# Optimization experiments

Hardware: AMD Instinct MI355X
Metric: run time of the kernel (lower is better)

Reference implementation:

```python
import jax, jax.numpy as jnp
import numpy as np

N_HEAD, D_MODEL, D_K, D_V = 8, 128, 16, 16
EPS = 1e-5


def entmax15(x):
    # 1.5-entmax along last axis (Peters & Martins 2019, exact sort-based algo)
    x = x * 0.5
    x = x - jnp.max(x, axis=-1, keepdims=True)
    xs = jnp.flip(jnp.sort(x, axis=-1), axis=-1)  # descending
    K = x.shape[-1]
    rho = jnp.arange(1, K + 1, dtype=x.dtype)
    mean = jnp.cumsum(xs, axis=-1) / rho
    mean_sq = jnp.cumsum(xs * xs, axis=-1) / rho
    delta = (1.0 - rho * (mean_sq - mean * mean)) / rho
    tau = mean - jnp.sqrt(jnp.clip(delta, 0.0))
    support = jnp.sum(tau <= xs, axis=-1, keepdims=True)  # support size k*
    tau_star = jnp.take_along_axis(tau, support - 1, axis=-1)
    p = jnp.clip(x - tau_star, 0.0)
    return p * p


def layer_norm(x, gamma, beta):
    mu = jnp.mean(x, axis=-1, keepdims=True)
    var = jnp.mean((x - mu) ** 2, axis=-1, keepdims=True)
    return gamma * (x - mu) * jax.lax.rsqrt(var + EPS) + beta


def setup_inputs() -> dict:
    key = jax.random.key(0)
    ks = jax.random.split(key, 24)
    B, Lq, Lk, D = 4, 1024, 2048, D_MODEL
    s = 0.05
    f = jax.random.normal
    return {
        "q": f(ks[0], (B, Lq, D), jnp.float32),
        "k": f(ks[1], (B, Lk, D), jnp.float32),
        "v": f(ks[2], (B, Lk, D), jnp.float32),
        "v_2": f(ks[3], (B, Lq, D), jnp.float32),
        "W_Q": f(ks[4], (D, N_HEAD * D_K)) * s, "b_Q": f(ks[5], (N_HEAD * D_K,)) * s,
        "W_K": f(ks[6], (D, N_HEAD * D_K)) * s, "b_K": f(ks[7], (N_HEAD * D_K,)) * s,
        "W_V": f(ks[8], (D, N_HEAD * D_V)) * s, "b_V": f(ks[9], (N_HEAD * D_V,)) * s,
        "W_V2": f(ks[10], (D, N_HEAD * D_V)) * s, "b_V2": f(ks[11], (N_HEAD * D_V,)) * s,
        "W_O": f(ks[12], (N_HEAD * D_V, D)) * s, "b_O": f(ks[13], (D,)) * s,
        "W_O2": f(ks[14], (N_HEAD * D_V, D)) * s, "b_O2": f(ks[15], (D,)) * s,
        "W_R": f(ks[16], (D, D)) * s,
        "W_R2": f(ks[17], (D, D)) * s,
        "gamma": jnp.ones((D,), jnp.float32),
        "beta": jnp.zeros((D,), jnp.float32),
    }


def reference(q, k, v, v_2, W_Q, b_Q, W_K, b_K, W_V, b_V, W_V2, b_V2,
              W_O, b_O, W_O2, b_O2, W_R, W_R2, gamma, beta):
    B, Lq, _ = q.shape
    Lk = k.shape[1]
    Q = (q @ W_Q + b_Q).reshape(B, Lq, N_HEAD, D_K)
    Kh = (k @ W_K + b_K).reshape(B, Lk, N_HEAD, D_K)
    V = (v @ W_V + b_V).reshape(B, Lk, N_HEAD, D_V)
    V2 = (v_2 @ W_V2 + b_V2).reshape(B, Lq, N_HEAD, D_V)
    # scores: [B, H, Lq, Lk]
    scores = jnp.einsum('bqhd,bkhd->bhqk', Q, Kh) / np.float32(np.sqrt(D_K))
    A = entmax15(scores)                              # normalize over Lk
    A2 = entmax15(jnp.swapaxes(scores, -2, -1))       # normalize over Lq
    out = jnp.einsum('bhqk,bkhd->bqhd', A, V).reshape(B, Lq, N_HEAD * D_V)
    out2 = jnp.einsum('bhkq,bqhd->bkhd', A2, V2).reshape(B, Lk, N_HEAD * D_V)
    # dropout is identity in eval mode; both branches use the SAME layer_norm params (as in source)
    out = jax.nn.relu(layer_norm(out @ W_O + b_O + q @ W_R, gamma, beta))
    out2 = jax.nn.relu(layer_norm(out2 @ W_O2 + b_O2 + k @ W_R2, gamma, beta))
    return (out, out2, A, A2)
```

## Files before the change

### kernel.cpp

```cpp
#include <hip/hip_runtime.h>

__global__ __launch_bounds__(128) void proj_all_kernel(
    const float* __restrict__ q, const float* __restrict__ k,
    const float* __restrict__ v, const float* __restrict__ v2,
    const float* __restrict__ W_Q, const float* __restrict__ b_Q,
    const float* __restrict__ W_K, const float* __restrict__ b_K,
    const float* __restrict__ W_V, const float* __restrict__ b_V,
    const float* __restrict__ W_V2, const float* __restrict__ b_V2,
    float* __restrict__ Qp, float* __restrict__ Kp,
    float* __restrict__ Vp, float* __restrict__ V2p)
{
  __shared__ float xs[4][128];
  int blk = blockIdx.x;
  const float *X, *W, *B; float* Y; int L, chunked, rb;
  if (blk < 1024)      { X = q;  W = W_Q;  B = b_Q;  Y = Qp;  L = 1024; chunked = 1; rb = blk; }
  else if (blk < 3072) { X = k;  W = W_K;  B = b_K;  Y = Kp;  L = 2048; chunked = 1; rb = blk - 1024; }
  else if (blk < 5120) { X = v;  W = W_V;  B = b_V;  Y = Vp;  L = 2048; chunked = 0; rb = blk - 3072; }
  else                 { X = v2; W = W_V2; B = b_V2; Y = V2p; L = 1024; chunked = 0; rb = blk - 5120; }
  rb *= 4;
  int c = threadIdx.x;
#pragma unroll
  for (int i = 0; i < 4; ++i)
    xs[i][c] = X[(size_t)(rb + i) * 128 + c];
  __syncthreads();
  float b = B[c];
  float a0 = b, a1 = b, a2 = b, a3 = b;
#pragma unroll 8
  for (int d = 0; d < 128; ++d) {
    float w = W[d * 128 + c];
    a0 = fmaf(xs[0][d], w, a0);
    a1 = fmaf(xs[1][d], w, a1);
    a2 = fmaf(xs[2][d], w, a2);
    a3 = fmaf(xs[3][d], w, a3);
  }
  int h = c >> 4, dd = c & 15;
  float av[4] = { a0, a1, a2, a3 };
#pragma unroll
  for (int i = 0; i < 4; ++i) {
    int row = rb + i;
    int bb = row / L;
    int l  = row - bb * L;
    if (chunked)
      Y[(((size_t)(bb * 8 + h) * 4 + (dd >> 2)) * L + l) * 4 + (dd & 3)] = av[i];
    else
      Y[((size_t)(bb * 8 + h) * L + l) * 16 + dd] = av[i];
  }
}

static __device__ __forceinline__ float hstep(float f, float s1, float cnt)
{
  float arg = fmaf(-cnt, f, s1 * s1);
  return (arg > 0.f) ? f / (s1 + sqrtf(arg)) : f / (2.f * s1);
}

template<int LROW, int LCOL>
__global__ __launch_bounds__(256, 4) void attn_kernel(
    const float* __restrict__ RowM, const float* __restrict__ ColM,
    const float* __restrict__ ValM, float* __restrict__ Aout,
    float* __restrict__ OutWs)
{
  constexpr int J   = LCOL / 64;
  constexpr int CAP = 512;
  __shared__ float          sval[4][2][CAP];
  __shared__ unsigned short sidx[4][2][CAP];

  int ws   = threadIdx.x >> 6;
  int pid  = blockIdx.x * 4 + ws;
  int lane = threadIdx.x & 63;
  int half   = lane >> 5;
  int lane31 = lane & 31;
  int bh   = pid / (LROW / 2);
  int pr   = pid - bh * (LROW / 2);
  int row0 = pr * 2;
  int bb   = bh >> 3, h = bh & 7;

  float qf0[16], qf1[16];
  { const float* qb = RowM + (size_t)bh * LROW * 16;
#pragma unroll
    for (int d = 0; d < 16; ++d) {
      qf0[d] = qb[((size_t)(d >> 2) * LROW + row0)     * 4 + (d & 3)] * 0.125f;
      qf1[d] = qb[((size_t)(d >> 2) * LROW + row0 + 1) * 4 + (d & 3)] * 0.125f;
    } }

  float x0[J], x1[J];
  const float4* Cb = (const float4*)(ColM + (size_t)bh * LCOL * 16);
#pragma unroll
  for (int j = 0; j < J; ++j) {
    int kk = lane + 64 * j;
    float4 k0 = Cb[0 * LCOL + kk];
    float4 k1 = Cb[1 * LCOL + kk];
    float4 k2 = Cb[2 * LCOL + kk];
    float4 k3 = Cb[3 * LCOL + kk];
    float kf[16] = { k0.x, k0.y, k0.z, k0.w, k1.x, k1.y, k1.z, k1.w,
                     k2.x, k2.y, k2.z, k2.w, k3.x, k3.y, k3.z, k3.w };
    float s0 = 0.f, s1 = 0.f;
#pragma unroll
    for (int d = 0; d < 16; ++d) {
      s0 = fmaf(qf0[d], kf[d], s0);
      s1 = fmaf(qf1[d], kf[d], s1);
    }
    x0[j] = s0; x1[j] = s1;
  }

  float m0 = -1e30f, m1 = -1e30f;
#pragma unroll
  for (int j = 0; j < J; ++j) { m0 = fmaxf(m0, x0[j]); m1 = fmaxf(m1, x1[j]); }
#pragma unroll
  for (int off = 32; off >= 1; off >>= 1) {
    m0 = fmaxf(m0, __shfl_xor(m0, off));
    m1 = fmaxf(m1, __shfl_xor(m1, off));
  }

  float tau0 = m0 - 1.0f, tau1 = m1 - 1.0f;

  bool done0 = false, done1 = false;
  bool compactable = false;
  for (int it = 0; it < 24; ++it) {
    float a1 = 0.f, a2 = 0.f;
    float b1 = 0.f, b2 = 0.f;
    int ac = 0, bc = 0;
#pragma unroll
    for (int j = 0; j < J; ++j) {
      float t0 = x0[j] - tau0, r0 = fmaxf(t0, 0.f);
      a1 += r0; a2 = fmaf(r0, r0, a2);
      ac += __popcll(__ballot(t0 > 0.f));
      float t1 = x1[j] - tau1, r1 = fmaxf(t1, 0.f);
      b1 += r1; b2 = fmaf(r1, r1, b2);
      bc += __popcll(__ballot(t1 > 0.f));
    }
#pragma unroll
    for (int off = 32; off >= 1; off >>= 1) {
      a1 += __shfl_xor(a1, off); a2 += __shfl_xor(a2, off);
      b1 += __shfl_xor(b1, off); b2 += __shfl_xor(b2, off);
    }
    float f0 = a2 - 1.0f, f1 = b2 - 1.0f;
    bool g0 = !done0 && (f0 > 1e-6f) && (a1 > 1e-12f);
    bool g1 = !done1 && (f1 > 1e-6f) && (b1 > 1e-12f);
    if (g0) tau0 += hstep(f0, a1, (float)ac); else done0 = true;
    if (g1) tau1 += hstep(f1, b1, (float)bc); else done1 = true;
    if (ac <= CAP && bc <= CAP) { compactable = true; break; }
    if (done0 && done1) break;
  }

  float* arow = Aout + ((size_t)bh * LROW + row0) * LCOL;
  const float* Vb = ValM + (size_t)bh * LCOL * 16;
  float* op = OutWs + ((size_t)bb * LROW + row0) * 128 + h * 16;

  if (compactable) {
    int c0 = 0, c1 = 0;
#pragma unroll
    for (int j = 0; j < J; ++j) {
      c0 += (x0[j] > tau0) ? 1 : 0;
      c1 += (x1[j] > tau1) ? 1 : 0;
    }
    int i0 = c0, i1 = c1;
#pragma unroll
    for (int off = 1; off <= 32; off <<= 1) {
      int t0 = __shfl_up(i0, off);
      int t1 = __shfl_up(i1, off);
      if (lane >= off) { i0 += t0; i1 += t1; }
    }
    int base0 = i0 - c0, base1 = i1 - c1;
    int tot0 = __shfl(i0, 63), tot1 = __shfl(i1, 63);
    int w0 = 0, w1 = 0;
#pragma unroll
    for (int j = 0; j < J; ++j) {
      if (x0[j] > tau0) {
        sval[ws][0][base0 + w0] = x0[j];
        sidx[ws][0][base0 + w0] = (unsigned short)(lane + 64 * j);
        ++w0;
      }
      if (x1[j] > tau1) {
        sval[ws][1][base1 + w1] = x1[j];
        sidx[ws][1][base1 + w1] = (unsigned short)(lane + 64 * j);
        ++w1;
      }
    }
    __threadfence_block();

    const float*          svp = &sval[ws][half][0];
    const unsigned short* sip = &sidx[ws][half][0];
    int   tot_my  = half ? tot1 : tot0;
    float tau_my  = half ? tau1 : tau0;
    bool  done_my = half ? done1 : done0;
    if (!(done0 && done1)) {
      for (int it = 0; it < 24; ++it) {
        float s1 = 0.f, s2 = 0.f, cm = 0.f;
        for (int i = lane31; i < tot_my; i += 32) {
          float t = svp[i] - tau_my, r = fmaxf(t, 0.f);
          s1 += r; s2 = fmaf(r, r, s2); cm += (t > 0.f) ? 1.f : 0.f;
        }
#pragma unroll
        for (int off = 16; off >= 1; off >>= 1) {
          s1 += __shfl_xor(s1, off);
          s2 += __shfl_xor(s2, off);
          cm += __shfl_xor(cm, off);
        }
        float f = s2 - 1.0f;
        bool g = !done_my && (f > 1e-6f) && (s1 > 1e-12f);
        if (g) tau_my += hstep(f, s1, cm); else done_my = true;
        if (__ballot(done_my) == ~0ull) break;
      }
    }
    tau0 = __shfl(tau_my, 0);
    tau1 = __shfl(tau_my, 32);

#pragma unroll
    for (int j = 0; j < J; ++j) {
      int kk = lane + 64 * j;
      float t0 = fmaxf(x0[j] - tau0, 0.f);
      float t1 = fmaxf(x1[j] - tau1, 0.f);
      arow[kk]        = t0 * t0;
      arow[LCOL + kk] = t1 * t1;
    }

    float acc[16];
#pragma unroll
    for (int d = 0; d < 16; ++d) acc[d] = 0.f;
    for (int i = lane31; i < tot_my; i += 32) {
      float t = svp[i] - tau_my;
      if (t > 0.f) {
        float p = t * t;
        int kk = sip[i];
        const float4* vp = (const float4*)(Vb + (size_t)kk * 16);
        float4 v0 = vp[0], v1 = vp[1], v2 = vp[2], v3 = vp[3];
        float vf[16] = { v0.x, v0.y, v0.z, v0.w, v1.x, v1.y, v1.z, v1.w,
                         v2.x, v2.y, v2.z, v2.w, v3.x, v3.y, v3.z, v3.w };
#pragma unroll
        for (int d = 0; d < 16; ++d) acc[d] = fmaf(p, vf[d], acc[d]);
      }
    }
#pragma unroll
    for (int off = 16; off >= 1; off >>= 1)
#pragma unroll
      for (int d = 0; d < 16; ++d) acc[d] += __shfl_xor(acc[d], off);
    float vv = acc[0];
#pragma unroll
    for (int d = 1; d < 16; ++d)
      vv = ((lane & 15) == d) ? acc[d] : vv;
    if (lane31 < 16) op[half * 128 + lane31] = vv;
    return;
  }

#pragma unroll
  for (int pass = 0; pass < 2; ++pass) {
    float taup = pass ? tau1 : tau0;
    float acc[16];
#pragma unroll
    for (int d = 0; d < 16; ++d) acc[d] = 0.f;
#pragma unroll
    for (int j = 0; j < J; ++j) {
      int kk = lane + 64 * j;
      float xv = pass ? x1[j] : x0[j];
      float t = fmaxf(xv - taup, 0.f), p = t * t;
      arow[(size_t)pass * LCOL + kk] = p;
      const float4* vp = (const float4*)(Vb + (size_t)kk * 16);
      float4 v0 = vp[0], v1 = vp[1], v2 = vp[2], v3 = vp[3];
      float vf[16] = { v0.x, v0.y, v0.z, v0.w, v1.x, v1.y, v1.z, v1.w,
                       v2.x, v2.y, v2.z, v2.w, v3.x, v3.y, v3.z, v3.w };
#pragma unroll
      for (int d = 0; d < 16; ++d) acc[d] = fmaf(p, vf[d], acc[d]);
    }
#pragma unroll
    for (int off = 32; off >= 1; off >>= 1)
#pragma unroll
      for (int d = 0; d < 16; ++d) acc[d] += __shfl_xor(acc[d], off);
    float vv = acc[0];
#pragma unroll
    for (int d = 1; d < 16; ++d)
      vv = (lane == d) ? acc[d] : vv;
    if (lane < 16) op[pass * 128 + lane] = vv;
  }
}

__global__ __launch_bounds__(128) void combine_ln_kernel(
    const float* __restrict__ X1, const float* __restrict__ X2,
    const float* __restrict__ W1, const float* __restrict__ W2,
    const float* __restrict__ bias, const float* __restrict__ gamma,
    const float* __restrict__ beta, float* __restrict__ O)
{
  __shared__ float x1s[4][128], x2s[4][128];
  __shared__ float red[2][8];
  int rb = blockIdx.x * 4;
  int c  = threadIdx.x;
#pragma unroll
  for (int i = 0; i < 4; ++i) {
    x1s[i][c] = X1[(size_t)(rb + i) * 128 + c];
    x2s[i][c] = X2[(size_t)(rb + i) * 128 + c];
  }
  __syncthreads();
  float b = bias[c];
  float a0 = b, a1 = b, a2 = b, a3 = b;
#pragma unroll 4
  for (int d = 0; d < 128; ++d) {
    float w1 = W1[d * 128 + c];
    float w2 = W2[d * 128 + c];
    a0 = fmaf(x1s[0][d], w1, fmaf(x2s[0][d], w2, a0));
    a1 = fmaf(x1s[1][d], w1, fmaf(x2s[1][d], w2, a1));
    a2 = fmaf(x1s[2][d], w1, fmaf(x2s[2][d], w2, a2));
    a3 = fmaf(x1s[3][d], w1, fmaf(x2s[3][d], w2, a3));
  }
  float s0 = a0, s1 = a1, s2 = a2, s3 = a3;
  float q0 = a0 * a0, q1 = a1 * a1, q2 = a2 * a2, q3 = a3 * a3;
#pragma unroll
  for (int off = 32; off >= 1; off >>= 1) {
    s0 += __shfl_xor(s0, off); q0 += __shfl_xor(q0, off);
    s1 += __shfl_xor(s1, off); q1 += __shfl_xor(q1, off);
    s2 += __shfl_xor(s2, off); q2 += __shfl_xor(q2, off);
    s3 += __shfl_xor(s3, off); q3 += __shfl_xor(q3, off);
  }
  int wv = c >> 6;
  if ((c & 63) == 0) {
    red[wv][0] = s0; red[wv][1] = q0; red[wv][2] = s1; red[wv][3] = q1;
    red[wv][4] = s2; red[wv][5] = q2; red[wv][6] = s3; red[wv][7] = q3;
  }
  __syncthreads();
  float S0 = red[0][0] + red[1][0], Q0 = red[0][1] + red[1][1];
  float S1 = red[0][2] + red[1][2], Q1 = red[0][3] + red[1][3];
  float S2 = red[0][4] + red[1][4], Q2 = red[0][5] + red[1][5];
  float S3 = red[0][6] + red[1][6], Q3 = red[0][7] + red[1][7];
  float g = gamma[c], be = beta[c];
  float mu, var, rs;
  mu = S0 * (1.f / 128.f); var = fmaxf(Q0 * (1.f / 128.f) - mu * mu, 0.f);
  rs = rsqrtf(var + 1e-5f);
  O[(size_t)(rb + 0) * 128 + c] = fmaxf(fmaf((a0 - mu) * rs, g, be), 0.f);
  mu = S1 * (1.f / 128.f); var = fmaxf(Q1 * (1.f / 128.f) - mu * mu, 0.f);
  rs = rsqrtf(var + 1e-5f);
  O[(size_t)(rb + 1) * 128 + c] = fmaxf(fmaf((a1 - mu) * rs, g, be), 0.f);
  mu = S2 * (1.f / 128.f); var = fmaxf(Q2 * (1.f / 128.f) - mu * mu, 0.f);
  rs = rsqrtf(var + 1e-5f);
  O[(size_t)(rb + 2) * 128 + c] = fmaxf(fmaf((a2 - mu) * rs, g, be), 0.f);
  mu = S3 * (1.f / 128.f); var = fmaxf(Q3 * (1.f / 128.f) - mu * mu, 0.f);
  rs = rsqrtf(var + 1e-5f);
  O[(size_t)(rb + 3) * 128 + c] = fmaxf(fmaf((a3 - mu) * rs, g, be), 0.f);
}

extern "C"
__attribute__((visibility("default"), used))
void kernel_launch(void* const* d_in, const int* in_sizes, int n_in,
                   void* d_out, int out_size, void* d_ws, size_t ws_size,
                   hipStream_t stream)
{
  (void)in_sizes; (void)n_in; (void)out_size; (void)ws_size;
  const float* q     = (const float*)d_in[0];
  const float* k     = (const float*)d_in[1];
  const float* v     = (const float*)d_in[2];
  const float* v2    = (const float*)d_in[3];
  const float* W_Q   = (const float*)d_in[4];
  const float* b_Q   = (const float*)d_in[5];
  const float* W_K   = (const float*)d_in[6];
  const float* b_K   = (const float*)d_in[7];
  const float* W_V   = (const float*)d_in[8];
  const float* b_V   = (const float*)d_in[9];
  const float* W_V2  = (const float*)d_in[10];
  const float* b_V2  = (const float*)d_in[11];
  const float* W_O   = (const float*)d_in[12];
  const float* b_O   = (const float*)d_in[13];
  const float* W_O2  = (const float*)d_in[14];
  const float* b_O2  = (const float*)d_in[15];
  const float* W_R   = (const float*)d_in[16];
  const float* W_R2  = (const float*)d_in[17];
  const float* gamma = (const float*)d_in[18];
  const float* beta  = (const float*)d_in[19];

  char* ws = (char*)d_ws;
  const size_t MB = 1u << 20;
  float* Qp    = (float*)(ws + 0);
  float* Kp    = (float*)(ws + 2 * MB);
  float* Vp    = (float*)(ws + 6 * MB);
  float* V2p   = (float*)(ws + 10 * MB);
  float* outm1 = (float*)(ws + 12 * MB);
  float* outm2 = (float*)(ws + 14 * MB);

  float* out1  = (float*)d_out;
  float* out2  = out1 + (size_t)524288;
  float* Aout  = out1 + (size_t)1572864;
  float* A2out = out1 + (size_t)68681728;

  proj_all_kernel<<<6144, 128, 0, stream>>>(
      q, k, v, v2, W_Q, b_Q, W_K, b_K, W_V, b_V, W_V2, b_V2,
      Qp, Kp, Vp, V2p);

  attn_kernel<1024, 2048><<<4096, 256, 0, stream>>>(Qp, Kp, Vp,  Aout,  outm1);
  attn_kernel<2048, 1024><<<8192, 256, 0, stream>>>(Kp, Qp, V2p, A2out, outm2);

  combine_ln_kernel<<<1024, 128, 0, stream>>>(outm1, q, W_O,  W_R,  b_O,
                                              gamma, beta, out1);
  combine_ln_kernel<<<2048, 128, 0, stream>>>(outm2, k, W_O2, W_R2, b_O2,
                                              gamma, beta, out2);
}
```

Baseline: 1.191 ms.

## Process one attention row per wavefront instead of two to raise occupancy

```diff
diff --git a/kernel.cpp b/kernel.cpp
--- a/kernel.cpp
+++ b/kernel.cpp
@@ -54,223 +54,196 @@
 }
 
 template<int LROW, int LCOL>
-__global__ __launch_bounds__(256, 4) void attn_kernel(
+__global__ __launch_bounds__(256, 6) void attn_kernel(
     const float* __restrict__ RowM, const float* __restrict__ ColM,
     const float* __restrict__ ValM, float* __restrict__ Aout,
     float* __restrict__ OutWs)
 {
   constexpr int J   = LCOL / 64;
   constexpr int CAP = 512;
-  __shared__ float          sval[4][2][CAP];
-  __shared__ unsigned short sidx[4][2][CAP];
+  __shared__ float          sval[4][CAP];
+  __shared__ unsigned short sidx[4][CAP];
 
   int ws   = threadIdx.x >> 6;
-  int pid  = blockIdx.x * 4 + ws;
+  int wid  = blockIdx.x * 4 + ws;
   int lane = threadIdx.x & 63;
-  int half   = lane >> 5;
-  int lane31 = lane & 31;
-  int bh   = pid / (LROW / 2);
-  int pr   = pid - bh * (LROW / 2);
-  int row0 = pr * 2;
+  int bh   = wid / LROW;
+  int r    = wid - bh * LROW;
   int bb   = bh >> 3, h = bh & 7;
 
-  float qf0[16], qf1[16];
+  float qf[16];
   { const float* qb = RowM + (size_t)bh * LROW * 16;
 #pragma unroll
-    for (int d = 0; d < 16; ++d) {
-      qf0[d] = qb[((size_t)(d >> 2) * LROW + row0)     * 4 + (d & 3)] * 0.125f;
-      qf1[d] = qb[((size_t)(d >> 2) * LROW + row0 + 1) * 4 + (d & 3)] * 0.125f;
-    } }
-
-  float x0[J], x1[J];
+    for (int d = 0; d < 16; ++d)
+      qf[d] = qb[((size_t)(d >> 2) * LROW + r) * 4 + (d & 3)] * 0.125f;
+  }
+
+  float x[J];
   const float4* Cb = (const float4*)(ColM + (size_t)bh * LCOL * 16);
 #pragma unroll
   for (int j = 0; j < J; ++j) {
     int kk = lane + 64 * j;
     float4 k0 = Cb[0 * LCOL + kk];
+    float  s  = qf[0] * k0.x;
+    s = fmaf(qf[1], k0.y, s); s = fmaf(qf[2], k0.z, s); s = fmaf(qf[3], k0.w, s);
     float4 k1 = Cb[1 * LCOL + kk];
+    s = fmaf(qf[4], k1.x, s); s = fmaf(qf[5], k1.y, s);
+    s = fmaf(qf[6], k1.z, s); s = fmaf(qf[7], k1.w, s);
     float4 k2 = Cb[2 * LCOL + kk];
+    s = fmaf(qf[8], k2.x, s); s = fmaf(qf[9], k2.y, s);
+    s = fmaf(qf[10], k2.z, s); s = fmaf(qf[11], k2.w, s);
     float4 k3 = Cb[3 * LCOL + kk];
-    float kf[16] = { k0.x, k0.y, k0.z, k0.w, k1.x, k1.y, k1.z, k1.w,
-                     k2.x, k2.y, k2.z, k2.w, k3.x, k3.y, k3.z, k3.w };
-    float s0 = 0.f, s1 = 0.f;
-#pragma unroll
-    for (int d = 0; d < 16; ++d) {
-      s0 = fmaf(qf0[d], kf[d], s0);
-      s1 = fmaf(qf1[d], kf[d], s1);
-    }
-    x0[j] = s0; x1[j] = s1;
-  }
-
-  float m0 = -1e30f, m1 = -1e30f;
-#pragma unroll
-  for (int j = 0; j < J; ++j) { m0 = fmaxf(m0, x0[j]); m1 = fmaxf(m1, x1[j]); }
-#pragma unroll
-  for (int off = 32; off >= 1; off >>= 1) {
-    m0 = fmaxf(m0, __shfl_xor(m0, off));
-    m1 = fmaxf(m1, __shfl_xor(m1, off));
-  }
-
-  float tau0 = m0 - 1.0f, tau1 = m1 - 1.0f;
-
-  bool done0 = false, done1 = false;
+    s = fmaf(qf[12], k3.x, s); s = fmaf(qf[13], k3.y, s);
+    s = fmaf(qf[14], k3.z, s); s = fmaf(qf[15], k3.w, s);
+    x[j] = s;
+  }
+
+  float m = -1e30f;
+#pragma unroll
+  for (int j = 0; j < J; ++j) m = fmaxf(m, x[j]);
+#pragma unroll
+  for (int off = 32; off >= 1; off >>= 1)
+    m = fmaxf(m, __shfl_xor(m, off));
+
+  float tau = m - 1.0f;
+
+  bool done = false;
   bool compactable = false;
   for (int it = 0; it < 24; ++it) {
     float a1 = 0.f, a2 = 0.f;
-    float b1 = 0.f, b2 = 0.f;
-    int ac = 0, bc = 0;
+    int ac = 0;
 #pragma unroll
     for (int j = 0; j < J; ++j) {
-      float t0 = x0[j] - tau0, r0 = fmaxf(t0, 0.f);
+      float t = x[j] - tau, r0 = fmaxf(t, 0.f);
       a1 += r0; a2 = fmaf(r0, r0, a2);
-      ac += __popcll(__ballot(t0 > 0.f));
-      float t1 = x1[j] - tau1, r1 = fmaxf(t1, 0.f);
-      b1 += r1; b2 = fmaf(r1, r1, b2);
-      bc += __popcll(__ballot(t1 > 0.f));
+      ac += __popcll(__ballot(t > 0.f));
     }
 #pragma unroll
     for (int off = 32; off >= 1; off >>= 1) {
-      a1 += __shfl_xor(a1, off); a2 += __shfl_xor(a2, off);
-      b1 += __shfl_xor(b1, off); b2 += __shfl_xor(b2, off);
-    }
-    float f0 = a2 - 1.0f, f1 = b2 - 1.0f;
-    bool g0 = !done0 && (f0 > 1e-6f) && (a1 > 1e-12f);
-    bool g1 = !done1 && (f1 > 1e-6f) && (b1 > 1e-12f);
-    if (g0) tau0 += hstep(f0, a1, (float)ac); else done0 = true;
-    if (g1) tau1 += hstep(f1, b1, (float)bc); else done1 = true;
-    if (ac <= CAP && bc <= CAP) { compactable = true; break; }
-    if (done0 && done1) break;
-  }
-
-  float* arow = Aout + ((size_t)bh * LROW + row0) * LCOL;
+      a1 += __shfl_xor(a1, off);
+      a2 += __shfl_xor(a2, off);
+    }
+    float f = a2 - 1.0f;
+    bool g = !done && (f > 1e-6f) && (a1 > 1e-12f);
+    if (g) tau += hstep(f, a1, (float)ac); else done = true;
+    if (ac <= CAP) { compactable = true; break; }
+    if (done) break;
+  }
+
+  float* arow = Aout + ((size_t)bh * LROW + r) * LCOL;
   const float* Vb = ValM + (size_t)bh * LCOL * 16;
-  float* op = OutWs + ((size_t)bb * LROW + row0) * 128 + h * 16;
+  float* op = OutWs + ((size_t)bb * LROW + r) * 128 + h * 16;
 
   if (compactable) {
-    int c0 = 0, c1 = 0;
+    int c = 0;
+#pragma unroll
+    for (int j = 0; j < J; ++j) c += (x[j] > tau) ? 1 : 0;
+    int i = c;
+#pragma unroll
+    for (int off = 1; off <= 32; off <<= 1) {
+      int t = __shfl_up(i, off);
+      if (lane >= off) i += t;
+    }
+    int base = i - c;
+    int tot  = __shfl(i, 63);
+    int w = 0;
 #pragma unroll
     for (int j = 0; j < J; ++j) {
-      c0 += (x0[j] > tau0) ? 1 : 0;
-      c1 += (x1[j] > tau1) ? 1 : 0;
-    }
-    int i0 = c0, i1 = c1;
-#pragma unroll
-    for (int off = 1; off <= 32; off <<= 1) {
-      int t0 = __shfl_up(i0, off);
-      int t1 = __shfl_up(i1, off);
-      if (lane >= off) { i0 += t0; i1 += t1; }
-    }
-    int base0 = i0 - c0, base1 = i1 - c1;
-    int tot0 = __shfl(i0, 63), tot1 = __shfl(i1, 63);
-    int w0 = 0, w1 = 0;
-#pragma unroll
-    for (int j = 0; j < J; ++j) {
-      if (x0[j] > tau0) {
-        sval[ws][0][base0 + w0] = x0[j];
-        sidx[ws][0][base0 + w0] = (unsigned short)(lane + 64 * j);
-        ++w0;
+      if (x[j] > tau) {
+        sval[ws][base + w] = x[j];
+        sidx[ws][base + w] = (unsigned short)(lane + 64 * j);
+        ++w;
       }
-      if (x1[j] > tau1) {
-        sval[ws][1][base1 + w1] = x1[j];
-        sidx[ws][1][base1 + w1] = (unsigned short)(lane + 64 * j);
-        ++w1;
-      }
     }
     __threadfence_block();
 
-    const float*          svp = &sval[ws][half][0];
-    const unsigned short* sip = &sidx[ws][half][0];
-    int   tot_my  = half ? tot1 : tot0;
-    float tau_my  = half ? tau1 : tau0;
-    bool  done_my = half ? done1 : done0;
-    if (!(done0 && done1)) {
+    if (!done) {
       for (int it = 0; it < 24; ++it) {
-        float s1 = 0.f, s2 = 0.f, cm = 0.f;
-        for (int i = lane31; i < tot_my; i += 32) {
-          float t = svp[i] - tau_my, r = fmaxf(t, 0.f);
-          s1 += r; s2 = fmaf(r, r, s2); cm += (t > 0.f) ? 1.f : 0.f;
+        float s1 = 0.f, s2 = 0.f;
+        int cnt = 0;
+        for (int i2 = lane; i2 < tot; i2 += 64) {
+          float t = sval[ws][i2] - tau, r0 = fmaxf(t, 0.f);
+          s1 += r0; s2 = fmaf(r0, r0, s2);
+          cnt += __popcll(__ballot(t > 0.f));
         }
 #pragma unroll
-        for (int off = 16; off >= 1; off >>= 1) {
+        for (int off = 32; off >= 1; off >>= 1) {
           s1 += __shfl_xor(s1, off);
           s2 += __shfl_xor(s2, off);
-          cm += __shfl_xor(cm, off);
         }
         float f = s2 - 1.0f;
-        bool g = !done_my && (f > 1e-6f) && (s1 > 1e-12f);
-        if (g) tau_my += hstep(f, s1, cm); else done_my = true;
-        if (__ballot(done_my) == ~0ull) break;
+        bool g = (f > 1e-6f) && (s1 > 1e-12f);
+        if (g) tau += hstep(f, s1, (float)cnt); else { done = true; break; }
       }
     }
-    tau0 = __shfl(tau_my, 0);
-    tau1 = __shfl(tau_my, 32);
 
 #pragma unroll
     for (int j = 0; j < J; ++j) {
       int kk = lane + 64 * j;
-      float t0 = fmaxf(x0[j] - tau0, 0.f);
-      float t1 = fmaxf(x1[j] - tau1, 0.f);
-      arow[kk]        = t0 * t0;
-      arow[LCOL + kk] = t1 * t1;
+      float t = fmaxf(x[j] - tau, 0.f);
+      arow[kk] = t * t;
     }
 
     float acc[16];
 #pragma unroll
     for (int d = 0; d < 16; ++d) acc[d] = 0.f;
-    for (int i = lane31; i < tot_my; i += 32) {
-      float t = svp[i] - tau_my;
+    for (int i2 = lane; i2 < tot; i2 += 64) {
+      float t = sval[ws][i2] - tau;
       if (t > 0.f) {
         float p = t * t;
-        int kk = sip[i];
+        int kk = sidx[ws][i2];
         const float4* vp = (const float4*)(Vb + (size_t)kk * 16);
         float4 v0 = vp[0], v1 = vp[1], v2 = vp[2], v3 = vp[3];
-        float vf[16] = { v0.x, v0.y, v0.z, v0.w, v1.x, v1.y, v1.z, v1.w,
-                         v2.x, v2.y, v2.z, v2.w, v3.x, v3.y, v3.z, v3.w };
-#pragma unroll
-        for (int d = 0; d < 16; ++d) acc[d] = fmaf(p, vf[d], acc[d]);
+        acc[0]  = fmaf(p, v0.x, acc[0]);  acc[1]  = fmaf(p, v0.y, acc[1]);
+        acc[2]  = fmaf(p, v0.z, acc[2]);  acc[3]  = fmaf(p, v0.w, acc[3]);
+        acc[4]  = fmaf(p, v1.x, acc[4]);  acc[5]  = fmaf(p, v1.y, acc[5]);
+        acc[6]  = fmaf(p, v1.z, acc[6]);  acc[7]  = fmaf(p, v1.w, acc[7]);
+        acc[8]  = fmaf(p, v2.x, acc[8]);  acc[9]  = fmaf(p, v2.y, acc[9]);
+        acc[10] = fmaf(p, v2.z, acc[10]); acc[11] = fmaf(p, v2.w, acc[11]);
+        acc[12] = fmaf(p, v3.x, acc[12]); acc[13] = fmaf(p, v3.y, acc[13]);
+        acc[14] = fmaf(p, v3.z, acc[14]); acc[15] = fmaf(p, v3.w, acc[15]);
       }
     }
 #pragma unroll
-    for (int off = 16; off >= 1; off >>= 1)
+    for (int off = 32; off >= 1; off >>= 1)
 #pragma unroll
       for (int d = 0; d < 16; ++d) acc[d] += __shfl_xor(acc[d], off);
     float vv = acc[0];
 #pragma unroll
     for (int d = 1; d < 16; ++d)
-      vv = ((lane & 15) == d) ? acc[d] : vv;
-    if (lane31 < 16) op[half * 128 + lane31] = vv;
+      vv = (lane == d) ? acc[d] : vv;
+    if (lane < 16) op[lane] = vv;
     return;
   }
 
-#pragma unroll
-  for (int pass = 0; pass < 2; ++pass) {
-    float taup = pass ? tau1 : tau0;
-    float acc[16];
-#pragma unroll
-    for (int d = 0; d < 16; ++d) acc[d] = 0.f;
-#pragma unroll
-    for (int j = 0; j < J; ++j) {
-      int kk = lane + 64 * j;
-      float xv = pass ? x1[j] : x0[j];
-      float t = fmaxf(xv - taup, 0.f), p = t * t;
-      arow[(size_t)pass * LCOL + kk] = p;
-      const float4* vp = (const float4*)(Vb + (size_t)kk * 16);
-      float4 v0 = vp[0], v1 = vp[1], v2 = vp[2], v3 = vp[3];
-      float vf[16] = { v0.x, v0.y, v0.z, v0.w, v1.x, v1.y, v1.z, v1.w,
-                       v2.x, v2.y, v2.z, v2.w, v3.x, v3.y, v3.z, v3.w };
-#pragma unroll
-      for (int d = 0; d < 16; ++d) acc[d] = fmaf(p, vf[d], acc[d]);
-    }
-#pragma unroll
-    for (int off = 32; off >= 1; off >>= 1)
-#pragma unroll
-      for (int d = 0; d < 16; ++d) acc[d] += __shfl_xor(acc[d], off);
-    float vv = acc[0];
-#pragma unroll
-    for (int d = 1; d < 16; ++d)
-      vv = (lane == d) ? acc[d] : vv;
-    if (lane < 16) op[pass * 128 + lane] = vv;
-  }
+  float acc[16];
+#pragma unroll
+  for (int d = 0; d < 16; ++d) acc[d] = 0.f;
+#pragma unroll
+  for (int j = 0; j < J; ++j) {
+    int kk = lane + 64 * j;
+    float t = fmaxf(x[j] - tau, 0.f), p = t * t;
+    arow[kk] = p;
+    const float4* vp = (const float4*)(Vb + (size_t)kk * 16);
+    float4 v0 = vp[0], v1 = vp[1], v2 = vp[2], v3 = vp[3];
+    acc[0]  = fmaf(p, v0.x, acc[0]);  acc[1]  = fmaf(p, v0.y, acc[1]);
+    acc[2]  = fmaf(p, v0.z, acc[2]);  acc[3]  = fmaf(p, v0.w, acc[3]);
+    acc[4]  = fmaf(p, v1.x, acc[4]);  acc[5]  = fmaf(p, v1.y, acc[5]);
+    acc[6]  = fmaf(p, v1.z, acc[6]);  acc[7]  = fmaf(p, v1.w, acc[7]);
+    acc[8]  = fmaf(p, v2.x, acc[8]);  acc[9]  = fmaf(p, v2.y, acc[9]);
+    acc[10] = fmaf(p, v2.z, acc[10]); acc[11] = fmaf(p, v2.w, acc[11]);
+    acc[12] = fmaf(p, v3.x, acc[12]); acc[13] = fmaf(p, v3.y, acc[13]);
+    acc[14] = fmaf(p, v3.z, acc[14]); acc[15] = fmaf(p, v3.w, acc[15]);
+  }
+#pragma unroll
+  for (int off = 32; off >= 1; off >>= 1)
+#pragma unroll
+    for (int d = 0; d < 16; ++d) acc[d] += __shfl_xor(acc[d], off);
+  float vv = acc[0];
+#pragma unroll
+  for (int d = 1; d < 16; ++d)
+    vv = (lane == d) ? acc[d] : vv;
+  if (lane < 16) op[lane] = vv;
 }
 
 __global__ __launch_bounds__(128) void combine_ln_kernel(
@@ -381,8 +354,8 @@
       q, k, v, v2, W_Q, b_Q, W_K, b_K, W_V, b_V, W_V2, b_V2,
       Qp, Kp, Vp, V2p);
 
-  attn_kernel<1024, 2048><<<4096, 256, 0, stream>>>(Qp, Kp, Vp,  Aout,  outm1);
-  attn_kernel<2048, 1024><<<8192, 256, 0, stream>>>(Kp, Qp, V2p, A2out, outm2);
+  attn_kernel<1024, 2048><<<8192,  256, 0, stream>>>(Qp, Kp, Vp,  Aout,  outm1);
+  attn_kernel<2048, 1024><<<16384, 256, 0, stream>>>(Kp, Qp, V2p, A2out, outm2);
 
   combine_ln_kernel<<<1024, 128, 0, stream>>>(outm1, q, W_O,  W_R,  b_O,
                                               gamma, beta, out1);
```

Result: slower. 1.489 ms (+25.1%).
